# Performance work log

Measured on AMD Instinct MI355X. Metric: run time of the kernel, lower is better.

The kernel has to match this reference:

```python
import jax, jax.numpy as jnp
import numpy as np

N = 100000   # nodes
E = 3200000  # edges
CIN = 6
H = 256
G = 16       # graphs in batch
EPS = 1e-5


def setup_inputs() -> dict:
    key = jax.random.key(0)
    ks = jax.random.split(key, 16)
    inp = {
        'pos': jax.random.normal(ks[0], (N, 3), dtype=jnp.float32),
        'norm': jax.random.normal(ks[1], (N, 3), dtype=jnp.float32),
        'edge_index': jax.random.randint(ks[2], (2, E), 0, N, dtype=jnp.int64),
        'batch': jnp.sort(jax.random.randint(ks[3], (N,), 0, G, dtype=jnp.int64)),
        'bn0_g': jnp.ones((CIN,), jnp.float32), 'bn0_b': jnp.zeros((CIN,), jnp.float32),
    }
    dims = [(CIN, H), (H, H), (H, H), (H, H)]
    for i, (ci, co) in enumerate(dims, start=1):
        inp[f'W{i}'] = jax.random.normal(ks[3 + i], (ci, co), jnp.float32) * 0.05
        inp[f'b{i}'] = jnp.zeros((co,), jnp.float32)
        inp[f'bn{i}_g'] = jnp.ones((co,), jnp.float32)
        inp[f'bn{i}_b'] = jnp.zeros((co,), jnp.float32)
    return inp


def _bn(x, g, b):
    # BatchNorm1d, training mode: biased batch stats over node dim
    m = jnp.mean(x, axis=0)
    v = jnp.var(x, axis=0)
    return (x - m) * jax.lax.rsqrt(v + EPS) * g + b


def _gcn(x, W, bias, row, col, en, sl):
    # GCNConv: linear -> symmetric-normalized aggregation (with self loops) -> +bias
    xw = x @ W                                             # [N, C_out]
    agg = jax.ops.segment_sum(en[:, None] * xw[row], col, num_segments=N)
    return agg + sl[:, None] * xw + bias


def reference(pos, norm, edge_index, batch,
              bn0_g, bn0_b,
              W1, b1, bn1_g, bn1_b,
              W2, b2, bn2_g, bn2_b,
              W3, b3, bn3_g, bn3_b,
              W4, b4, bn4_g, bn4_b):
    row, col = edge_index[0], edge_index[1]
    # gcn_norm with self loops: deg includes +1 self loop weight
    deg = jax.ops.segment_sum(jnp.ones((E,), jnp.float32), col, num_segments=N) + 1.0
    dinv = jax.lax.rsqrt(deg)
    en = dinv[row] * dinv[col]   # edge norm
    sl = dinv * dinv             # self-loop norm

    x = jnp.concatenate([pos, norm], axis=1)   # [N, 6]
    x = _bn(x, bn0_g, bn0_b)
    for (W, b, g, be) in [(W1, b1, bn1_g, bn1_b), (W2, b2, bn2_g, bn2_b),
                          (W3, b3, bn3_g, bn3_b), (W4, b4, bn4_g, bn4_b)]:
        x = _bn(jax.nn.relu(_gcn(x, W, b, row, col, en, sl)), g, be)

    # global mean pool over graph ids
    sums = jax.ops.segment_sum(x, batch, num_segments=G)
    cnt = jax.ops.segment_sum(jnp.ones((N,), jnp.float32), batch, num_segments=G)
    return sums / jnp.maximum(cnt, 1.0)[:, None]
```

## Files before the change

kernel.cpp:

```cpp
#include <hip/hip_runtime.h>
#include <hip/hip_bf16.h>
#include <cstdint>

#define N_NODES 100000
#define NPAD    100032
#define N_EDGES 3200000
#define HID 256
#define NG 16
#define BN_EPS 1e-5f
#define B0 120
#define PB 1024
#define SROWS ((N_NODES + PB - 1) / PB)
#define PBR 128
#define RPR (PB / PBR)
#define FPART 25000
#define LDSROW 264

typedef unsigned short u16;
using bf16x8 = __attribute__((ext_vector_type(8))) short;
using f32x4  = __attribute__((ext_vector_type(4))) float;

__device__ __forceinline__ float bf2f(u16 b) {
    return __uint_as_float(((unsigned)b) << 16);
}
__device__ __forceinline__ u16 f2bf(float f) {
    unsigned u = __float_as_uint(f);
    unsigned r = (u + 0x7FFFu + ((u >> 16) & 1u)) >> 16;
    return (u16)r;
}
__device__ __forceinline__ float4 ld_bf16x4(const u16* p) {
    ushort4 u = *reinterpret_cast<const ushort4*>(p);
    float4 f;
    f.x = bf2f(u.x); f.y = bf2f(u.y); f.z = bf2f(u.z); f.w = bf2f(u.w);
    return f;
}

__global__ void k_count(const int* __restrict__ coli, int* __restrict__ cnt) {
    int i = blockIdx.x * blockDim.x + threadIdx.x;
    int st = gridDim.x * blockDim.x;
    for (; i < N_EDGES; i += st) atomicAdd(&cnt[coli[i]], 1);
}

__global__ void k_scan(const int* __restrict__ cnt, int* __restrict__ ptr,
                       int* __restrict__ ptr2, float* __restrict__ dinv) {
    __shared__ int wsum[16];
    const int t = threadIdx.x;
    const int wv = t >> 6;
    const int ln = t & 63;
    int carry = 0;
    for (int base = 0; base < N_NODES; base += 4096) {
        int idx = base + t * 4;
        int v0 = 0, v1 = 0, v2 = 0, v3 = 0;
        if (idx + 3 < N_NODES) {
            int4 q = *reinterpret_cast<const int4*>(&cnt[idx]);
            v0 = q.x; v1 = q.y; v2 = q.z; v3 = q.w;
        } else {
            if (idx + 0 < N_NODES) v0 = cnt[idx + 0];
            if (idx + 1 < N_NODES) v1 = cnt[idx + 1];
            if (idx + 2 < N_NODES) v2 = cnt[idx + 2];
        }
        if (idx + 0 < N_NODES) dinv[idx + 0] = rsqrtf((float)v0 + 1.0f);
        if (idx + 1 < N_NODES) dinv[idx + 1] = rsqrtf((float)v1 + 1.0f);
        if (idx + 2 < N_NODES) dinv[idx + 2] = rsqrtf((float)v2 + 1.0f);
        if (idx + 3 < N_NODES) dinv[idx + 3] = rsqrtf((float)v3 + 1.0f);
        int s = v0 + v1 + v2 + v3;
        int sc = s;
        for (int off = 1; off < 64; off <<= 1) {
            int u = __shfl_up(sc, off);
            if (ln >= off) sc += u;
        }
        if (ln == 63) wsum[wv] = sc;
        __syncthreads();
        if (wv == 0 && ln < 16) {
            int a = wsum[ln];
            for (int off = 1; off < 16; off <<= 1) {
                int u = __shfl_up(a, off, 16);
                if (ln >= off) a += u;
            }
            wsum[ln] = a;
        }
        __syncthreads();
        int total = wsum[15];
        int excl = carry + (wv ? wsum[wv - 1] : 0) + sc - s;
        if (idx + 0 < N_NODES) { ptr[idx + 0] = excl; ptr2[idx + 0] = excl; } excl += v0;
        if (idx + 1 < N_NODES) { ptr[idx + 1] = excl; ptr2[idx + 1] = excl; } excl += v1;
        if (idx + 2 < N_NODES) { ptr[idx + 2] = excl; ptr2[idx + 2] = excl; } excl += v2;
        if (idx + 3 < N_NODES) { ptr[idx + 3] = excl; ptr2[idx + 3] = excl; }
        __syncthreads();
        carry += total;
    }
    if (t == 0) ptr[N_NODES] = carry;
}

__global__ void k_fillp(const int* __restrict__ rowi, const int* __restrict__ coli,
                        int* __restrict__ ptr2, int* __restrict__ esrc, int lo) {
    int i = blockIdx.x * blockDim.x + threadIdx.x;
    int st = gridDim.x * blockDim.x;
    const int hi = lo + FPART;
    for (; i < N_EDGES; i += st) {
        int c = coli[i];
        if (c >= lo && c < hi) {
            int r = rowi[i];
            int p = atomicAdd(&ptr2[c], 1);
            esrc[p] = r;
        }
    }
}

__global__ __launch_bounds__(256) void k_bn0stats(const float* __restrict__ pos,
                                                  const float* __restrict__ nrm,
                                                  const int* __restrict__ batch,
                                                  float* __restrict__ part ,
                                                  int* __restrict__ cg) {
    __shared__ int h[NG];
    if (threadIdx.x < NG) h[threadIdx.x] = 0;
    __syncthreads();
    float s[6] = {0, 0, 0, 0, 0, 0}, q[6] = {0, 0, 0, 0, 0, 0};
    int i = blockIdx.x * blockDim.x + threadIdx.x;
    int stp = gridDim.x * blockDim.x;
    for (; i < N_NODES; i += stp) {
        float v;
        v = pos[i * 3 + 0]; s[0] += v; q[0] += v * v;
        v = pos[i * 3 + 1]; s[1] += v; q[1] += v * v;
        v = pos[i * 3 + 2]; s[2] += v; q[2] += v * v;
        v = nrm[i * 3 + 0]; s[3] += v; q[3] += v * v;
        v = nrm[i * 3 + 1]; s[4] += v; q[4] += v * v;
        v = nrm[i * 3 + 2]; s[5] += v; q[5] += v * v;
        atomicAdd(&h[batch[i]], 1);
    }
#pragma unroll
    for (int k = 0; k < 6; ++k) {
        for (int o = 32; o > 0; o >>= 1) { s[k] += __shfl_down(s[k], o); q[k] += __shfl_down(q[k], o); }
    }
    __shared__ float ls[4][12];
    const int wv = threadIdx.x >> 6;
    const int ln = threadIdx.x & 63;
    if (ln == 0) {
#pragma unroll
        for (int k = 0; k < 6; ++k) { ls[wv][k] = s[k]; ls[wv][6 + k] = q[k]; }
    }
    __syncthreads();
    if (threadIdx.x < 12)
        part[blockIdx.x * 12 + threadIdx.x] =
            ls[0][threadIdx.x] + ls[1][threadIdx.x] + ls[2][threadIdx.x] + ls[3][threadIdx.x];
    if (threadIdx.x < NG) {
        int v = h[threadIdx.x];
        if (v) atomicAdd(&cg[threadIdx.x], v);
    }
}

__global__ void k_fold6(const float* __restrict__ W,
                        const float* __restrict__ part, float invcnt,
                        const float* __restrict__ gamma, const float* __restrict__ beta,
                        float* __restrict__ Wf, float* __restrict__ rvB) {
    __shared__ float st[12];
    int c = threadIdx.x;
    if (c < 12) {
        float a = 0.f;
        for (int b = 0; b < B0; ++b) a += part[b * 12 + c];
        st[c] = a;
    }
    __syncthreads();
    float acc = 0.f;
    for (int k = 0; k < 6; ++k) {
        float m = st[k] * invcnt;
        float var = st[6 + k] * invcnt - m * m;
        float A = gamma[k] * rsqrtf(var + BN_EPS);
        float B = beta[k] - m * A;
        float w = W[k * HID + c];
        Wf[k * HID + c] = A * w;
        acc = fmaf(B, w, acc);
    }
    rvB[c] = acc;
}

__global__ __launch_bounds__(256) void k_reduce(const float* __restrict__ part,
                                                float* __restrict__ red) {
    const int b = blockIdx.x;
    const int t = threadIdx.x;
    float a0 = 0.f, a1 = 0.f;
#pragma unroll
    for (int r = 0; r < RPR; ++r) {
        const float* p = &part[(size_t)(b * RPR + r) * 512];
        a0 += p[t];
        a1 += p[t + 256];
    }
    red[(size_t)b * 512 + t] = a0;
    red[(size_t)b * 512 + 256 + t] = a1;
}

__global__ void k_fold256(const float* __restrict__ W,
                          const float* __restrict__ red , float invcnt,
                          const float* __restrict__ gamma, const float* __restrict__ beta,
                          u16* __restrict__ WhiT, u16* __restrict__ WloT,
                          float* __restrict__ rv) {
    __shared__ float ss[HID], sq[HID];
    int c = threadIdx.x;
    {
        float a = 0.f, b = 0.f;
#pragma unroll 4
        for (int bb = 0; bb < PBR; ++bb) {
            a += red[bb * 512 + c];
            b += red[bb * 512 + HID + c];
        }
        ss[c] = a; sq[c] = b;
    }
    __syncthreads();
    float acc = 0.f;
    for (int k = 0; k < HID; ++k) {
        float m = ss[k] * invcnt;
        float var = sq[k] * invcnt - m * m;
        float A = gamma[k] * rsqrtf(var + BN_EPS);
        float B = beta[k] - m * A;
        float w = W[k * HID + c];
        float wf = A * w;
        u16 hi = f2bf(wf);
        WhiT[c * HID + k] = hi;
        WloT[c * HID + k] = f2bf(wf - bf2f(hi));
        acc = fmaf(B, w, acc);
    }
    rv[c] = acc;
}

__global__ __launch_bounds__(256) void k_l1fused(
    const float* __restrict__ pos, const float* __restrict__ nrm,
    const int* __restrict__ ptr, const int* __restrict__ esrc,
    const float* __restrict__ dinv, const float* __restrict__ Wf,
    const float* __restrict__ rvB, const float* __restrict__ b1,
    u16* __restrict__ out) {
    const int wv = threadIdx.x >> 6;
    const int ln = threadIdx.x & 63;
    float w[6][4], rv4[4], bb4[4];
#pragma unroll
    for (int k = 0; k < 6; ++k) {
        float4 t = *reinterpret_cast<const float4*>(&Wf[k * HID + ln * 4]);
        w[k][0] = t.x; w[k][1] = t.y; w[k][2] = t.z; w[k][3] = t.w;
    }
    {
        float4 t = *reinterpret_cast<const float4*>(&rvB[ln * 4]);
        rv4[0] = t.x; rv4[1] = t.y; rv4[2] = t.z; rv4[3] = t.w;
        float4 u = *reinterpret_cast<const float4*>(&b1[ln * 4]);
        bb4[0] = u.x; bb4[1] = u.y; bb4[2] = u.z; bb4[3] = u.w;
    }
    for (int n = blockIdx.x * 4 + wv; n < N_NODES; n += gridDim.x * 4) {
        const float dn = dinv[n];
        float z0 = 0, z1 = 0, z2 = 0, z3 = 0, z4 = 0, z5 = 0, t = 0;
        const int s_ = ptr[n], e_ = ptr[n + 1];
        for (int e = s_ + ln; e < e_; e += 64) {
            int src = esrc[e];
            float we = dn * dinv[src];
            z0 = fmaf(we, pos[src * 3 + 0], z0);
            z1 = fmaf(we, pos[src * 3 + 1], z1);
            z2 = fmaf(we, pos[src * 3 + 2], z2);
            z3 = fmaf(we, nrm[src * 3 + 0], z3);
            z4 = fmaf(we, nrm[src * 3 + 1], z4);
            z5 = fmaf(we, nrm[src * 3 + 2], z5);
            t += we;
        }
        if (ln == 0) {
            float sl = dn * dn;
            z0 = fmaf(sl, pos[n * 3 + 0], z0);
            z1 = fmaf(sl, pos[n * 3 + 1], z1);
            z2 = fmaf(sl, pos[n * 3 + 2], z2);
            z3 = fmaf(sl, nrm[n * 3 + 0], z3);
            z4 = fmaf(sl, nrm[n * 3 + 1], z4);
            z5 = fmaf(sl, nrm[n * 3 + 2], z5);
            t += sl;
        }
#pragma unroll
        for (int o = 1; o < 64; o <<= 1) {
            z0 += __shfl_xor(z0, o); z1 += __shfl_xor(z1, o); z2 += __shfl_xor(z2, o);
            z3 += __shfl_xor(z3, o); z4 += __shfl_xor(z4, o); z5 += __shfl_xor(z5, o);
            t  += __shfl_xor(t, o);
        }
        ushort4 o4;
        float oj;
        oj = fmaf(t, rv4[0], bb4[0]);
        oj = fmaf(z0, w[0][0], oj); oj = fmaf(z1, w[1][0], oj); oj = fmaf(z2, w[2][0], oj);
        oj = fmaf(z3, w[3][0], oj); oj = fmaf(z4, w[4][0], oj); oj = fmaf(z5, w[5][0], oj);
        o4.x = f2bf(fmaxf(oj, 0.f));
        oj = fmaf(t, rv4[1], bb4[1]);
        oj = fmaf(z0, w[0][1], oj); oj = fmaf(z1, w[1][1], oj); oj = fmaf(z2, w[2][1], oj);
        oj = fmaf(z3, w[3][1], oj); oj = fmaf(z4, w[4][1], oj); oj = fmaf(z5, w[5][1], oj);
        o4.y = f2bf(fmaxf(oj, 0.f));
        oj = fmaf(t, rv4[2], bb4[2]);
        oj = fmaf(z0, w[0][2], oj); oj = fmaf(z1, w[1][2], oj); oj = fmaf(z2, w[2][2], oj);
        oj = fmaf(z3, w[3][2], oj); oj = fmaf(z4, w[4][2], oj); oj = fmaf(z5, w[5][2], oj);
        o4.z = f2bf(fmaxf(oj, 0.f));
        oj = fmaf(t, rv4[3], bb4[3]);
        oj = fmaf(z0, w[0][3], oj); oj = fmaf(z1, w[1][3], oj); oj = fmaf(z2, w[2][3], oj);
        oj = fmaf(z3, w[3][3], oj); oj = fmaf(z4, w[4][3], oj); oj = fmaf(z5, w[5][3], oj);
        o4.w = f2bf(fmaxf(oj, 0.f));
        *reinterpret_cast<ushort4*>(&out[(size_t)n * HID + ln * 4]) = o4;
    }
}

__global__ __launch_bounds__(256) void k_gemm_lds(
    const u16* __restrict__ X, const u16* __restrict__ WhiT,
    const u16* __restrict__ WloT, const float* __restrict__ rv,
    u16* __restrict__ out) {
    __shared__ u16 As[64 * LDSROW];
    const int tid = threadIdx.x;
    const int wv = tid >> 6;
    const int ln = tid & 63;
    const int row0 = blockIdx.x * 64;
    const int lr = ln & 15;
    const int lk = (ln >> 4) * 8;
    const int wcol0 = wv * 64;

#pragma unroll
    for (int i = 0; i < 8; ++i) {
        int chunk = i * 256 + tid;
        int r = chunk >> 5;
        int kc = chunk & 31;
        bf16x8 v = *reinterpret_cast<const bf16x8*>(&X[(size_t)(row0 + r) * HID + kc * 8]);
        *reinterpret_cast<bf16x8*>(&As[r * LDSROW + kc * 8]) = v;
    }
    __syncthreads();

    f32x4 acc[4][4] = {};
    for (int kk = 0; kk < HID; kk += 32) {
        bf16x8 a[4], bh[4], bl[4];
#pragma unroll
        for (int i = 0; i < 4; ++i)
            a[i] = *reinterpret_cast<const bf16x8*>(&As[(i * 16 + lr) * LDSROW + kk + lk]);
#pragma unroll
        for (int c = 0; c < 4; ++c) {
            int col = wcol0 + c * 16 + lr;
            bh[c] = *reinterpret_cast<const bf16x8*>(&WhiT[(size_t)col * HID + kk + lk]);
            bl[c] = *reinterpret_cast<const bf16x8*>(&WloT[(size_t)col * HID + kk + lk]);
        }
#pragma unroll
        for (int i = 0; i < 4; ++i)
#pragma unroll
            for (int c = 0; c < 4; ++c) {
                acc[i][c] = __builtin_amdgcn_mfma_f32_16x16x32_bf16(a[i], bh[c], acc[i][c], 0, 0, 0);
                acc[i][c] = __builtin_amdgcn_mfma_f32_16x16x32_bf16(a[i], bl[c], acc[i][c], 0, 0, 0);
            }
    }
    const int crow = (ln >> 4) * 4;
#pragma unroll
    for (int c = 0; c < 4; ++c) {
        int col = wcol0 + c * 16 + lr;
        float rvc = rv[col];
#pragma unroll
        for (int i = 0; i < 4; ++i) {
#pragma unroll
            for (int rg = 0; rg < 4; ++rg) {
                int r = row0 + i * 16 + crow + rg;
                out[(size_t)r * HID + col] = f2bf(acc[i][c][rg] + rvc);
            }
        }
    }
}

__global__ __launch_bounds__(256) void k_agg(
    const u16* __restrict__ xw, const int* __restrict__ ptr,
    const int* __restrict__ esrc, const float* __restrict__ dinv,
    const float* __restrict__ bias, u16* __restrict__ y) {
    const int wv = threadIdx.x >> 6;
    const int ln = threadIdx.x & 63;
    const int n = blockIdx.x * 4 + wv;
    const float dn = dinv[n];
    const size_t base = (size_t)n * HID + ln * 4;
    float4 v = ld_bf16x4(&xw[base]);
    const float sl = dn * dn;
    float a0 = v.x * sl, a1 = v.y * sl, a2 = v.z * sl, a3 = v.w * sl;
    const int s = ptr[n], e = ptr[n + 1];
    for (int bs = s; bs < e; bs += 64) {
        const int cnt = (e - bs < 64) ? e - bs : 64;
        int myidx = 0;
        float myw = 0.f;
        if (ln < cnt) {
            myidx = esrc[bs + ln];
            myw = dinv[myidx] * dn;
        }
        int j = 0;
        for (; j + 7 < cnt; j += 8) {
            int   s0 = __shfl(myidx, j),     s1 = __shfl(myidx, j + 1);
            int   s2 = __shfl(myidx, j + 2), s3 = __shfl(myidx, j + 3);
            int   s4 = __shfl(myidx, j + 4), s5 = __shfl(myidx, j + 5);
            int   s6 = __shfl(myidx, j + 6), s7 = __shfl(myidx, j + 7);
            float w0 = __shfl(myw, j),       w1 = __shfl(myw, j + 1);
            float w2 = __shfl(myw, j + 2),   w3 = __shfl(myw, j + 3);
            float w4 = __shfl(myw, j + 4),   w5 = __shfl(myw, j + 5);
            float w6 = __shfl(myw, j + 6),   w7 = __shfl(myw, j + 7);
            float4 u0 = ld_bf16x4(&xw[(size_t)s0 * HID + ln * 4]);
            float4 u1 = ld_bf16x4(&xw[(size_t)s1 * HID + ln * 4]);
            float4 u2 = ld_bf16x4(&xw[(size_t)s2 * HID + ln * 4]);
            float4 u3 = ld_bf16x4(&xw[(size_t)s3 * HID + ln * 4]);
            float4 u4 = ld_bf16x4(&xw[(size_t)s4 * HID + ln * 4]);
            float4 u5 = ld_bf16x4(&xw[(size_t)s5 * HID + ln * 4]);
            float4 u6 = ld_bf16x4(&xw[(size_t)s6 * HID + ln * 4]);
            float4 u7 = ld_bf16x4(&xw[(size_t)s7 * HID + ln * 4]);
            a0 = fmaf(w0, u0.x, a0); a1 = fmaf(w0, u0.y, a1);
            a2 = fmaf(w0, u0.z, a2); a3 = fmaf(w0, u0.w, a3);
            a0 = fmaf(w1, u1.x, a0); a1 = fmaf(w1, u1.y, a1);
            a2 = fmaf(w1, u1.z, a2); a3 = fmaf(w1, u1.w, a3);
            a0 = fmaf(w2, u2.x, a0); a1 = fmaf(w2, u2.y, a1);
            a2 = fmaf(w2, u2.z, a2); a3 = fmaf(w2, u2.w, a3);
            a0 = fmaf(w3, u3.x, a0); a1 = fmaf(w3, u3.y, a1);
            a2 = fmaf(w3, u3.z, a2); a3 = fmaf(w3, u3.w, a3);
            a0 = fmaf(w4, u4.x, a0); a1 = fmaf(w4, u4.y, a1);
            a2 = fmaf(w4, u4.z, a2); a3 = fmaf(w4, u4.w, a3);
            a0 = fmaf(w5, u5.x, a0); a1 = fmaf(w5, u5.y, a1);
            a2 = fmaf(w5, u5.z, a2); a3 = fmaf(w5, u5.w, a3);
            a0 = fmaf(w6, u6.x, a0); a1 = fmaf(w6, u6.y, a1);
            a2 = fmaf(w6, u6.z, a2); a3 = fmaf(w6, u6.w, a3);
            a0 = fmaf(w7, u7.x, a0); a1 = fmaf(w7, u7.y, a1);
            a2 = fmaf(w7, u7.z, a2); a3 = fmaf(w7, u7.w, a3);
        }
        for (; j < cnt; ++j) {
            int   s0 = __shfl(myidx, j);
            float w0 = __shfl(myw, j);
            float4 u0 = ld_bf16x4(&xw[(size_t)s0 * HID + ln * 4]);
            a0 = fmaf(w0, u0.x, a0); a1 = fmaf(w0, u0.y, a1);
            a2 = fmaf(w0, u0.z, a2); a3 = fmaf(w0, u0.w, a3);
        }
    }
    float4 b = *reinterpret_cast<const float4*>(&bias[ln * 4]);
    a0 = fmaxf(a0 + b.x, 0.f);
    a1 = fmaxf(a1 + b.y, 0.f);
    a2 = fmaxf(a2 + b.z, 0.f);
    a3 = fmaxf(a3 + b.w, 0.f);
    ushort4 o;
    o.x = f2bf(a0); o.y = f2bf(a1); o.z = f2bf(a2); o.w = f2bf(a3);
    *reinterpret_cast<ushort4*>(&y[base]) = o;
}

__global__ __launch_bounds__(256) void k_stats(const u16* __restrict__ y,
                                               float* __restrict__ part ) {
    const int t = threadIdx.x;
    const int cl = t & 63;
    const int rp = t >> 6;
    const int n0 = blockIdx.x * SROWS;
    const int n1 = (n0 + SROWS < N_NODES) ? n0 + SROWS : N_NODES;
    float s0 = 0, s1 = 0, s2 = 0, s3 = 0, q0 = 0, q1 = 0, q2 = 0, q3 = 0;
    for (int n = n0 + rp; n < n1; n += 4) {
        float4 v = ld_bf16x4(&y[(size_t)n * HID + cl * 4]);
        s0 += v.x; q0 = fmaf(v.x, v.x, q0);
        s1 += v.y; q1 = fmaf(v.y, v.y, q1);
        s2 += v.z; q2 = fmaf(v.z, v.z, q2);
        s3 += v.w; q3 = fmaf(v.w, v.w, q3);
    }
    __shared__ float sh[4 * 512];
    float* shr = &sh[rp * 512];
    shr[cl * 4 + 0] = s0; shr[cl * 4 + 1] = s1;
    shr[cl * 4 + 2] = s2; shr[cl * 4 + 3] = s3;
    shr[256 + cl * 4 + 0] = q0; shr[256 + cl * 4 + 1] = q1;
    shr[256 + cl * 4 + 2] = q2; shr[256 + cl * 4 + 3] = q3;
    __syncthreads();
    float a = sh[t] + sh[512 + t] + sh[1024 + t] + sh[1536 + t];
    float b = sh[256 + t] + sh[768 + t] + sh[1280 + t] + sh[1792 + t];
    part[blockIdx.x * 512 + t] = a;
    part[blockIdx.x * 512 + 256 + t] = b;
}

__global__ __launch_bounds__(256) void k_statspool(const u16* __restrict__ y,
                                                   const int* __restrict__ batch,
                                                   float* __restrict__ part,
                                                   float* __restrict__ ps) {
    const int c = threadIdx.x;
    const int n0 = blockIdx.x * SROWS;
    const int n1 = (n0 + SROWS < N_NODES) ? n0 + SROWS : N_NODES;
    float s = 0.f, q = 0.f;
    if (n0 < N_NODES) {
        int cur = batch[n0];
        float acc = 0.f;
        for (int n = n0; n < n1; ++n) {
            float v = bf2f(y[(size_t)n * HID + c]);
            int g = batch[n];
            if (g != cur) {
                atomicAdd(&ps[cur * HID + c], acc);
                acc = 0.f;
                cur = g;
            }
            s += v;
            q = fmaf(v, v, q);
            acc += v;
        }
        atomicAdd(&ps[cur * HID + c], acc);
    }
    part[blockIdx.x * 512 + c] = s;
    part[blockIdx.x * 512 + HID + c] = q;
}

__global__ void k_final(const float* __restrict__ ps, const int* __restrict__ cg,
                        const float* __restrict__ red, const float* __restrict__ gamma,
                        const float* __restrict__ beta, float* __restrict__ out) {
    __shared__ float ss[HID], sq[HID];
    const int c = threadIdx.x;
    {
        float a = 0.f, b = 0.f;
#pragma unroll 4
        for (int bb = 0; bb < PBR; ++bb) {
            a += red[bb * 512 + c];
            b += red[bb * 512 + HID + c];
        }
        ss[c] = a; sq[c] = b;
    }
    __syncthreads();
    const float invn = 1.0f / (float)N_NODES;
    float m = ss[c] * invn;
    float var = sq[c] * invn - m * m;
    float A = gamma[c] * rsqrtf(var + BN_EPS);
    float B = beta[c] - m * A;
    for (int g = 0; g < NG; ++g) {
        float cn = (float)cg[g];
        float val = (A * ps[g * HID + c] + cn * B) / fmaxf(cn, 1.0f);
        out[g * HID + c] = val;
    }
}

extern "C" void kernel_launch(void* const* d_in, const int* in_sizes, int n_in,
                              void* d_out, int out_size, void* d_ws, size_t ws_size,
                              hipStream_t stream) {
    const float* pos   = (const float*)d_in[0];
    const float* nrm   = (const float*)d_in[1];
    const int*   ei    = (const int*)d_in[2];
    const int*   batch = (const int*)d_in[3];
    const float* bn0g  = (const float*)d_in[4];
    const float* bn0b  = (const float*)d_in[5];
    const float* W[4]   = {(const float*)d_in[6],  (const float*)d_in[10], (const float*)d_in[14], (const float*)d_in[18]};
    const float* bb[4]  = {(const float*)d_in[7],  (const float*)d_in[11], (const float*)d_in[15], (const float*)d_in[19]};
    const float* bg[4]  = {(const float*)d_in[8],  (const float*)d_in[12], (const float*)d_in[16], (const float*)d_in[20]};
    const float* bbt[4] = {(const float*)d_in[9],  (const float*)d_in[13], (const float*)d_in[17], (const float*)d_in[21]};

    char* wp = (char*)d_ws;
    auto alloc = [&](size_t bytes) {
        char* p = wp;
        wp += (bytes + 255) & ~(size_t)255;
        return p;
    };
    float* dinv  = (float*)alloc((size_t)N_NODES * 4);
    int*   cnt   = (int*)  alloc((size_t)N_NODES * 4);
    int*   ptr   = (int*)  alloc((size_t)(N_NODES + 1) * 4);
    int*   ptr2  = (int*)  alloc((size_t)N_NODES * 4);
    int*   esrc  = (int*)  alloc((size_t)N_EDGES * 4);
    u16*   bufA  = (u16*)  alloc((size_t)NPAD * HID * 2);
    u16*   bufB  = (u16*)  alloc((size_t)NPAD * HID * 2);
    float* part0 = (float*)alloc((size_t)B0 * 12 * 4);
    float* partL = (float*)alloc((size_t)PB * 512 * 4);
    float* red   = (float*)alloc((size_t)PBR * 512 * 4);
    float* Wf1   = (float*)alloc((size_t)6 * HID * 4);
    u16*   WhiT  = (u16*)  alloc((size_t)HID * HID * 2);
    u16*   WloT  = (u16*)  alloc((size_t)HID * HID * 2);
    float* rv    = (float*)alloc(HID * 4);
    float* psz   = (float*)alloc((size_t)(NG * HID + NG) * 4);
    float* ps    = psz;
    int*   cg    = (int*)(psz + NG * HID);
    (void)ws_size; (void)in_sizes; (void)n_in; (void)out_size;

    const int* rowi = ei;
    const int* coli = ei + N_EDGES;

    hipMemsetAsync(cnt, 0, (size_t)N_NODES * 4, stream);
    hipMemsetAsync(psz, 0, (size_t)(NG * HID + NG) * 4, stream);

    k_count<<<2048, 256, 0, stream>>>(coli, cnt);
    k_scan<<<1, 1024, 0, stream>>>(cnt, ptr, ptr2, dinv);
    for (int p = 0; p < 4; ++p)
        k_fillp<<<1024, 256, 0, stream>>>(rowi, coli, ptr2, esrc, p * FPART);

    k_bn0stats<<<B0, 256, 0, stream>>>(pos, nrm, batch, part0, cg);
    k_fold6<<<1, 256, 0, stream>>>(W[0], part0, 1.0f / (float)N_NODES, bn0g, bn0b, Wf1, rv);
    k_l1fused<<<2048, 256, 0, stream>>>(pos, nrm, ptr, esrc, dinv, Wf1, rv, bb[0], bufA);

    for (int l = 0; l < 3; ++l) {
        k_stats<<<PB, 256, 0, stream>>>(bufA, partL);
        k_reduce<<<PBR, 256, 0, stream>>>(partL, red);
        k_fold256<<<1, 256, 0, stream>>>(W[l + 1], red, 1.0f / (float)N_NODES,
                                         bg[l], bbt[l], WhiT, WloT, rv);
        k_gemm_lds<<<NPAD / 64, 256, 0, stream>>>(bufA, WhiT, WloT, rv, bufB);
        k_agg<<<N_NODES / 4, 256, 0, stream>>>(bufB, ptr, esrc, dinv, bb[l + 1], bufA);
    }

    k_statspool<<<PB, 256, 0, stream>>>(bufA, batch, partL, ps);
    k_reduce<<<PBR, 256, 0, stream>>>(partL, red);
    k_final<<<1, 256, 0, stream>>>(ps, cg, red, bg[3], bbt[3], (float*)d_out);
}
```

Baseline: 1.615 ms.

## Fuse BN statistics into aggregation kernels and parallelize the CSR scan

```diff
diff --git a/kernel.cpp b/kernel.cpp
--- a/kernel.cpp
+++ b/kernel.cpp
@@ -9,12 +9,12 @@
 #define NG 16
 #define BN_EPS 1e-5f
 #define B0 120
-#define PB 1024
-#define SROWS ((N_NODES + PB - 1) / PB)
-#define PBR 128
-#define RPR (PB / PBR)
+#define NB 391
+#define SLABS 128
 #define FPART 25000
 #define LDSROW 264
+#define AGB 2048
+#define NGRP (N_NODES / 4)
 
 typedef unsigned short u16;
 using bf16x8 = __attribute__((ext_vector_type(8))) short;
@@ -41,55 +41,55 @@
     for (; i < N_EDGES; i += st) atomicAdd(&cnt[coli[i]], 1);
 }
 
-__global__ void k_scan(const int* __restrict__ cnt, int* __restrict__ ptr,
-                       int* __restrict__ ptr2, float* __restrict__ dinv) {
-    __shared__ int wsum[16];
+__global__ __launch_bounds__(256) void k_scanA(const int* __restrict__ cnt,
+                                               int* __restrict__ bsum) {
     const int t = threadIdx.x;
-    const int wv = t >> 6;
-    const int ln = t & 63;
-    int carry = 0;
-    for (int base = 0; base < N_NODES; base += 4096) {
-        int idx = base + t * 4;
-        int v0 = 0, v1 = 0, v2 = 0, v3 = 0;
-        if (idx + 3 < N_NODES) {
-            int4 q = *reinterpret_cast<const int4*>(&cnt[idx]);
-            v0 = q.x; v1 = q.y; v2 = q.z; v3 = q.w;
-        } else {
-            if (idx + 0 < N_NODES) v0 = cnt[idx + 0];
-            if (idx + 1 < N_NODES) v1 = cnt[idx + 1];
-            if (idx + 2 < N_NODES) v2 = cnt[idx + 2];
-        }
-        if (idx + 0 < N_NODES) dinv[idx + 0] = rsqrtf((float)v0 + 1.0f);
-        if (idx + 1 < N_NODES) dinv[idx + 1] = rsqrtf((float)v1 + 1.0f);
-        if (idx + 2 < N_NODES) dinv[idx + 2] = rsqrtf((float)v2 + 1.0f);
-        if (idx + 3 < N_NODES) dinv[idx + 3] = rsqrtf((float)v3 + 1.0f);
-        int s = v0 + v1 + v2 + v3;
-        int sc = s;
-        for (int off = 1; off < 64; off <<= 1) {
-            int u = __shfl_up(sc, off);
-            if (ln >= off) sc += u;
-        }
-        if (ln == 63) wsum[wv] = sc;
-        __syncthreads();
-        if (wv == 0 && ln < 16) {
-            int a = wsum[ln];
-            for (int off = 1; off < 16; off <<= 1) {
-                int u = __shfl_up(a, off, 16);
-                if (ln >= off) a += u;
-            }
-            wsum[ln] = a;
-        }
-        __syncthreads();
-        int total = wsum[15];
-        int excl = carry + (wv ? wsum[wv - 1] : 0) + sc - s;
-        if (idx + 0 < N_NODES) { ptr[idx + 0] = excl; ptr2[idx + 0] = excl; } excl += v0;
-        if (idx + 1 < N_NODES) { ptr[idx + 1] = excl; ptr2[idx + 1] = excl; } excl += v1;
-        if (idx + 2 < N_NODES) { ptr[idx + 2] = excl; ptr2[idx + 2] = excl; } excl += v2;
-        if (idx + 3 < N_NODES) { ptr[idx + 3] = excl; ptr2[idx + 3] = excl; }
-        __syncthreads();
-        carry += total;
-    }
-    if (t == 0) ptr[N_NODES] = carry;
+    const int i = blockIdx.x * 256 + t;
+    int v = (i < N_NODES) ? cnt[i] : 0;
+    for (int o = 32; o > 0; o >>= 1) v += __shfl_down(v, o);
+    __shared__ int ws[4];
+    if ((t & 63) == 0) ws[t >> 6] = v;
+    __syncthreads();
+    if (t == 0) bsum[blockIdx.x] = ws[0] + ws[1] + ws[2] + ws[3];
+}
+
+__global__ __launch_bounds__(512) void k_scanB(const int* __restrict__ bsum,
+                                               int* __restrict__ boff,
+                                               int* __restrict__ ptrN) {
+    const int t = threadIdx.x;
+    const int ln = t & 63, wv = t >> 6;
+    int v = (t < NB) ? bsum[t] : 0;
+    int sc = v;
+    for (int o = 1; o < 64; o <<= 1) { int u = __shfl_up(sc, o); if (ln >= o) sc += u; }
+    __shared__ int ws[8], wx[9];
+    if (ln == 63) ws[wv] = sc;
+    __syncthreads();
+    if (t == 0) { int a = 0; for (int k = 0; k < 8; ++k) { wx[k] = a; a += ws[k]; } wx[8] = a; }
+    __syncthreads();
+    int excl = wx[wv] + sc - v;
+    if (t < NB) boff[t] = excl;
+    if (t == 0) ptrN[0] = wx[8];
+}
+
+__global__ __launch_bounds__(256) void k_scanC(const int* __restrict__ cnt,
+                                               const int* __restrict__ boff,
+                                               int* __restrict__ ptr,
+                                               int* __restrict__ ptr2,
+                                               float* __restrict__ dinv) {
+    const int t = threadIdx.x;
+    const int i = blockIdx.x * 256 + t;
+    const int ln = t & 63, wv = t >> 6;
+    int v = (i < N_NODES) ? cnt[i] : 0;
+    if (i < N_NODES) dinv[i] = rsqrtf((float)v + 1.0f);
+    int sc = v;
+    for (int o = 1; o < 64; o <<= 1) { int u = __shfl_up(sc, o); if (ln >= o) sc += u; }
+    __shared__ int ws[4], wx[4];
+    if (ln == 63) ws[wv] = sc;
+    __syncthreads();
+    if (t == 0) { int a = 0; for (int k = 0; k < 4; ++k) { wx[k] = a; a += ws[k]; } }
+    __syncthreads();
+    int excl = boff[blockIdx.x] + wx[wv] + sc - v;
+    if (i < N_NODES) { ptr[i] = excl; ptr2[i] = excl; }
 }
 
 __global__ void k_fillp(const int* __restrict__ rowi, const int* __restrict__ coli,
@@ -174,23 +174,8 @@
     rvB[c] = acc;
 }
 
-__global__ __launch_bounds__(256) void k_reduce(const float* __restrict__ part,
-                                                float* __restrict__ red) {
-    const int b = blockIdx.x;
-    const int t = threadIdx.x;
-    float a0 = 0.f, a1 = 0.f;
-#pragma unroll
-    for (int r = 0; r < RPR; ++r) {
-        const float* p = &part[(size_t)(b * RPR + r) * 512];
-        a0 += p[t];
-        a1 += p[t + 256];
-    }
-    red[(size_t)b * 512 + t] = a0;
-    red[(size_t)b * 512 + 256 + t] = a1;
-}
-
 __global__ void k_fold256(const float* __restrict__ W,
-                          const float* __restrict__ red , float invcnt,
+                          const float* __restrict__ partL , float invcnt,
                           const float* __restrict__ gamma, const float* __restrict__ beta,
                           u16* __restrict__ WhiT, u16* __restrict__ WloT,
                           float* __restrict__ rv) {
@@ -199,9 +184,9 @@
     {
         float a = 0.f, b = 0.f;
 #pragma unroll 4
-        for (int bb = 0; bb < PBR; ++bb) {
-            a += red[bb * 512 + c];
-            b += red[bb * 512 + HID + c];
+        for (int bb = 0; bb < SLABS; ++bb) {
+            a += partL[bb * 512 + c];
+            b += partL[bb * 512 + HID + c];
         }
         ss[c] = a; sq[c] = b;
     }
@@ -227,7 +212,7 @@
     const int* __restrict__ ptr, const int* __restrict__ esrc,
     const float* __restrict__ dinv, const float* __restrict__ Wf,
     const float* __restrict__ rvB, const float* __restrict__ b1,
-    u16* __restrict__ out) {
+    u16* __restrict__ out, float* __restrict__ partL) {
     const int wv = threadIdx.x >> 6;
     const int ln = threadIdx.x & 63;
     float w[6][4], rv4[4], bb4[4];
@@ -242,7 +227,8 @@
         float4 u = *reinterpret_cast<const float4*>(&b1[ln * 4]);
         bb4[0] = u.x; bb4[1] = u.y; bb4[2] = u.z; bb4[3] = u.w;
     }
-    for (int n = blockIdx.x * 4 + wv; n < N_NODES; n += gridDim.x * 4) {
+    float ssr[4] = {0, 0, 0, 0}, qqr[4] = {0, 0, 0, 0};
+    for (int n = blockIdx.x * 4 + wv; n < N_NODES; n += AGB * 4) {
         const float dn = dinv[n];
         float z0 = 0, z1 = 0, z2 = 0, z3 = 0, z4 = 0, z5 = 0, t = 0;
         const int s_ = ptr[n], e_ = ptr[n + 1];
@@ -274,25 +260,28 @@
             t  += __shfl_xor(t, o);
         }
         ushort4 o4;
-        float oj;
-        oj = fmaf(t, rv4[0], bb4[0]);
-        oj = fmaf(z0, w[0][0], oj); oj = fmaf(z1, w[1][0], oj); oj = fmaf(z2, w[2][0], oj);
-        oj = fmaf(z3, w[3][0], oj); oj = fmaf(z4, w[4][0], oj); oj = fmaf(z5, w[5][0], oj);
-        o4.x = f2bf(fmaxf(oj, 0.f));
-        oj = fmaf(t, rv4[1], bb4[1]);
-        oj = fmaf(z0, w[0][1], oj); oj = fmaf(z1, w[1][1], oj); oj = fmaf(z2, w[2][1], oj);
-        oj = fmaf(z3, w[3][1], oj); oj = fmaf(z4, w[4][1], oj); oj = fmaf(z5, w[5][1], oj);
-        o4.y = f2bf(fmaxf(oj, 0.f));
-        oj = fmaf(t, rv4[2], bb4[2]);
-        oj = fmaf(z0, w[0][2], oj); oj = fmaf(z1, w[1][2], oj); oj = fmaf(z2, w[2][2], oj);
-        oj = fmaf(z3, w[3][2], oj); oj = fmaf(z4, w[4][2], oj); oj = fmaf(z5, w[5][2], oj);
-        o4.z = f2bf(fmaxf(oj, 0.f));
-        oj = fmaf(t, rv4[3], bb4[3]);
-        oj = fmaf(z0, w[0][3], oj); oj = fmaf(z1, w[1][3], oj); oj = fmaf(z2, w[2][3], oj);
-        oj = fmaf(z3, w[3][3], oj); oj = fmaf(z4, w[4][3], oj); oj = fmaf(z5, w[5][3], oj);
-        o4.w = f2bf(fmaxf(oj, 0.f));
+#pragma unroll
+        for (int j = 0; j < 4; ++j) {
+            float oj = fmaf(t, rv4[j], bb4[j]);
+            oj = fmaf(z0, w[0][j], oj); oj = fmaf(z1, w[1][j], oj); oj = fmaf(z2, w[2][j], oj);
+            oj = fmaf(z3, w[3][j], oj); oj = fmaf(z4, w[4][j], oj); oj = fmaf(z5, w[5][j], oj);
+            oj = fmaxf(oj, 0.f);
+            ssr[j] += oj; qqr[j] = fmaf(oj, oj, qqr[j]);
+            ((u16*)&o4)[j] = f2bf(oj);
+        }
         *reinterpret_cast<ushort4*>(&out[(size_t)n * HID + ln * 4]) = o4;
     }
+    __shared__ float sh[4 * 512];
+    float* shw = &sh[wv * 512];
+#pragma unroll
+    for (int j = 0; j < 4; ++j) { shw[ln * 4 + j] = ssr[j]; shw[256 + ln * 4 + j] = qqr[j]; }
+    __syncthreads();
+    const int t = threadIdx.x;
+    float S = sh[t] + sh[512 + t] + sh[1024 + t] + sh[1536 + t];
+    float Q = sh[256 + t] + sh[768 + t] + sh[1280 + t] + sh[1792 + t];
+    float* slab = &partL[(size_t)(blockIdx.x & (SLABS - 1)) * 512];
+    atomicAdd(&slab[t], S);
+    atomicAdd(&slab[256 + t], Q);
 }
 
 __global__ __launch_bounds__(256) void k_gemm_lds(
@@ -357,145 +346,113 @@
 __global__ __launch_bounds__(256) void k_agg(
     const u16* __restrict__ xw, const int* __restrict__ ptr,
     const int* __restrict__ esrc, const float* __restrict__ dinv,
-    const float* __restrict__ bias, u16* __restrict__ y) {
+    const float* __restrict__ bias, u16* __restrict__ y,
+    float* __restrict__ partL) {
     const int wv = threadIdx.x >> 6;
     const int ln = threadIdx.x & 63;
-    const int n = blockIdx.x * 4 + wv;
-    const float dn = dinv[n];
-    const size_t base = (size_t)n * HID + ln * 4;
-    float4 v = ld_bf16x4(&xw[base]);
-    const float sl = dn * dn;
-    float a0 = v.x * sl, a1 = v.y * sl, a2 = v.z * sl, a3 = v.w * sl;
-    const int s = ptr[n], e = ptr[n + 1];
-    for (int bs = s; bs < e; bs += 64) {
-        const int cnt = (e - bs < 64) ? e - bs : 64;
-        int myidx = 0;
-        float myw = 0.f;
-        if (ln < cnt) {
-            myidx = esrc[bs + ln];
-            myw = dinv[myidx] * dn;
-        }
-        int j = 0;
-        for (; j + 7 < cnt; j += 8) {
-            int   s0 = __shfl(myidx, j),     s1 = __shfl(myidx, j + 1);
-            int   s2 = __shfl(myidx, j + 2), s3 = __shfl(myidx, j + 3);
-            int   s4 = __shfl(myidx, j + 4), s5 = __shfl(myidx, j + 5);
-            int   s6 = __shfl(myidx, j + 6), s7 = __shfl(myidx, j + 7);
-            float w0 = __shfl(myw, j),       w1 = __shfl(myw, j + 1);
-            float w2 = __shfl(myw, j + 2),   w3 = __shfl(myw, j + 3);
-            float w4 = __shfl(myw, j + 4),   w5 = __shfl(myw, j + 5);
-            float w6 = __shfl(myw, j + 6),   w7 = __shfl(myw, j + 7);
-            float4 u0 = ld_bf16x4(&xw[(size_t)s0 * HID + ln * 4]);
-            float4 u1 = ld_bf16x4(&xw[(size_t)s1 * HID + ln * 4]);
-            float4 u2 = ld_bf16x4(&xw[(size_t)s2 * HID + ln * 4]);
-            float4 u3 = ld_bf16x4(&xw[(size_t)s3 * HID + ln * 4]);
-            float4 u4 = ld_bf16x4(&xw[(size_t)s4 * HID + ln * 4]);
-            float4 u5 = ld_bf16x4(&xw[(size_t)s5 * HID + ln * 4]);
-            float4 u6 = ld_bf16x4(&xw[(size_t)s6 * HID + ln * 4]);
-            float4 u7 = ld_bf16x4(&xw[(size_t)s7 * HID + ln * 4]);
-            a0 = fmaf(w0, u0.x, a0); a1 = fmaf(w0, u0.y, a1);
-            a2 = fmaf(w0, u0.z, a2); a3 = fmaf(w0, u0.w, a3);
-            a0 = fmaf(w1, u1.x, a0); a1 = fmaf(w1, u1.y, a1);
-            a2 = fmaf(w1, u1.z, a2); a3 = fmaf(w1, u1.w, a3);
-            a0 = fmaf(w2, u2.x, a0); a1 = fmaf(w2, u2.y, a1);
-            a2 = fmaf(w2, u2.z, a2); a3 = fmaf(w2, u2.w, a3);
-            a0 = fmaf(w3, u3.x, a0); a1 = fmaf(w3, u3.y, a1);
-            a2 = fmaf(w3, u3.z, a2); a3 = fmaf(w3, u3.w, a3);
-            a0 = fmaf(w4, u4.x, a0); a1 = fmaf(w4, u4.y, a1);
-            a2 = fmaf(w4, u4.z, a2); a3 = fmaf(w4, u4.w, a3);
-            a0 = fmaf(w5, u5.x, a0); a1 = fmaf(w5, u5.y, a1);
-            a2 = fmaf(w5, u5.z, a2); a3 = fmaf(w5, u5.w, a3);
-            a0 = fmaf(w6, u6.x, a0); a1 = fmaf(w6, u6.y, a1);
-            a2 = fmaf(w6, u6.z, a2); a3 = fmaf(w6, u6.w, a3);
-            a0 = fmaf(w7, u7.x, a0); a1 = fmaf(w7, u7.y, a1);
-            a2 = fmaf(w7, u7.z, a2); a3 = fmaf(w7, u7.w, a3);
-        }
-        for (; j < cnt; ++j) {
-            int   s0 = __shfl(myidx, j);
-            float w0 = __shfl(myw, j);
-            float4 u0 = ld_bf16x4(&xw[(size_t)s0 * HID + ln * 4]);
-            a0 = fmaf(w0, u0.x, a0); a1 = fmaf(w0, u0.y, a1);
-            a2 = fmaf(w0, u0.z, a2); a3 = fmaf(w0, u0.w, a3);
-        }
-    }
     float4 b = *reinterpret_cast<const float4*>(&bias[ln * 4]);
-    a0 = fmaxf(a0 + b.x, 0.f);
-    a1 = fmaxf(a1 + b.y, 0.f);
-    a2 = fmaxf(a2 + b.z, 0.f);
-    a3 = fmaxf(a3 + b.w, 0.f);
-    ushort4 o;
-    o.x = f2bf(a0); o.y = f2bf(a1); o.z = f2bf(a2); o.w = f2bf(a3);
-    *reinterpret_cast<ushort4*>(&y[base]) = o;
-}
-
-__global__ __launch_bounds__(256) void k_stats(const u16* __restrict__ y,
-                                               float* __restrict__ part ) {
+    float ssr[4] = {0, 0, 0, 0}, qqr[4] = {0, 0, 0, 0};
+    for (int g = blockIdx.x; g < NGRP; g += AGB) {
+        const int n = g * 4 + wv;
+        const float dn = dinv[n];
+        const size_t base = (size_t)n * HID + ln * 4;
+        float4 v = ld_bf16x4(&xw[base]);
+        const float sl = dn * dn;
+        float a0 = v.x * sl, a1 = v.y * sl, a2 = v.z * sl, a3 = v.w * sl;
+        const int s = ptr[n], e = ptr[n + 1];
+        for (int bs = s; bs < e; bs += 64) {
+            const int cnt = (e - bs < 64) ? e - bs : 64;
+            int myidx = 0;
+            float myw = 0.f;
+            if (ln < cnt) {
+                myidx = esrc[bs + ln];
+                myw = dinv[myidx] * dn;
+            }
+            int j = 0;
+            for (; j + 3 < cnt; j += 4) {
+                int   s0 = __shfl(myidx, j),     s1 = __shfl(myidx, j + 1);
+                int   s2 = __shfl(myidx, j + 2), s3 = __shfl(myidx, j + 3);
+                float w0 = __shfl(myw, j),       w1 = __shfl(myw, j + 1);
+                float w2 = __shfl(myw, j + 2),   w3 = __shfl(myw, j + 3);
+                float4 u0 = ld_bf16x4(&xw[(size_t)s0 * HID + ln * 4]);
+                float4 u1 = ld_bf16x4(&xw[(size_t)s1 * HID + ln * 4]);
+                float4 u2 = ld_bf16x4(&xw[(size_t)s2 * HID + ln * 4]);
+                float4 u3 = ld_bf16x4(&xw[(size_t)s3 * HID + ln * 4]);
+                a0 = fmaf(w0, u0.x, a0); a1 = fmaf(w0, u0.y, a1);
+                a2 = fmaf(w0, u0.z, a2); a3 = fmaf(w0, u0.w, a3);
+                a0 = fmaf(w1, u1.x, a0); a1 = fmaf(w1, u1.y, a1);
+                a2 = fmaf(w1, u1.z, a2); a3 = fmaf(w1, u1.w, a3);
+                a0 = fmaf(w2, u2.x, a0); a1 = fmaf(w2, u2.y, a1);
+                a2 = fmaf(w2, u2.z, a2); a3 = fmaf(w2, u2.w, a3);
+                a0 = fmaf(w3, u3.x, a0); a1 = fmaf(w3, u3.y, a1);
+                a2 = fmaf(w3, u3.z, a2); a3 = fmaf(w3, u3.w, a3);
+            }
+            for (; j < cnt; ++j) {
+                int   s0 = __shfl(myidx, j);
+                float w0 = __shfl(myw, j);
+                float4 u0 = ld_bf16x4(&xw[(size_t)s0 * HID + ln * 4]);
+                a0 = fmaf(w0, u0.x, a0); a1 = fmaf(w0, u0.y, a1);
+                a2 = fmaf(w0, u0.z, a2); a3 = fmaf(w0, u0.w, a3);
+            }
+        }
+        a0 = fmaxf(a0 + b.x, 0.f);
+        a1 = fmaxf(a1 + b.y, 0.f);
+        a2 = fmaxf(a2 + b.z, 0.f);
+        a3 = fmaxf(a3 + b.w, 0.f);
+        ssr[0] += a0; qqr[0] = fmaf(a0, a0, qqr[0]);
+        ssr[1] += a1; qqr[1] = fmaf(a1, a1, qqr[1]);
+        ssr[2] += a2; qqr[2] = fmaf(a2, a2, qqr[2]);
+        ssr[3] += a3; qqr[3] = fmaf(a3, a3, qqr[3]);
+        ushort4 o;
+        o.x = f2bf(a0); o.y = f2bf(a1); o.z = f2bf(a2); o.w = f2bf(a3);
+        *reinterpret_cast<ushort4*>(&y[base]) = o;
+    }
+    __shared__ float sh[4 * 512];
+    float* shw = &sh[wv * 512];
+#pragma unroll
+    for (int j = 0; j < 4; ++j) { shw[ln * 4 + j] = ssr[j]; shw[256 + ln * 4 + j] = qqr[j]; }
+    __syncthreads();
     const int t = threadIdx.x;
-    const int cl = t & 63;
-    const int rp = t >> 6;
-    const int n0 = blockIdx.x * SROWS;
-    const int n1 = (n0 + SROWS < N_NODES) ? n0 + SROWS : N_NODES;
-    float s0 = 0, s1 = 0, s2 = 0, s3 = 0, q0 = 0, q1 = 0, q2 = 0, q3 = 0;
-    for (int n = n0 + rp; n < n1; n += 4) {
-        float4 v = ld_bf16x4(&y[(size_t)n * HID + cl * 4]);
-        s0 += v.x; q0 = fmaf(v.x, v.x, q0);
-        s1 += v.y; q1 = fmaf(v.y, v.y, q1);
-        s2 += v.z; q2 = fmaf(v.z, v.z, q2);
-        s3 += v.w; q3 = fmaf(v.w, v.w, q3);
-    }
-    __shared__ float sh[4 * 512];
-    float* shr = &sh[rp * 512];
-    shr[cl * 4 + 0] = s0; shr[cl * 4 + 1] = s1;
-    shr[cl * 4 + 2] = s2; shr[cl * 4 + 3] = s3;
-    shr[256 + cl * 4 + 0] = q0; shr[256 + cl * 4 + 1] = q1;
-    shr[256 + cl * 4 + 2] = q2; shr[256 + cl * 4 + 3] = q3;
-    __syncthreads();
-    float a = sh[t] + sh[512 + t] + sh[1024 + t] + sh[1536 + t];
-    float b = sh[256 + t] + sh[768 + t] + sh[1280 + t] + sh[1792 + t];
-    part[blockIdx.x * 512 + t] = a;
-    part[blockIdx.x * 512 + 256 + t] = b;
-}
-
-__global__ __launch_bounds__(256) void k_statspool(const u16* __restrict__ y,
-                                                   const int* __restrict__ batch,
-                                                   float* __restrict__ part,
-                                                   float* __restrict__ ps) {
+    float S = sh[t] + sh[512 + t] + sh[1024 + t] + sh[1536 + t];
+    float Q = sh[256 + t] + sh[768 + t] + sh[1280 + t] + sh[1792 + t];
+    float* slab = &partL[(size_t)(blockIdx.x & (SLABS - 1)) * 512];
+    atomicAdd(&slab[t], S);
+    atomicAdd(&slab[256 + t], Q);
+}
+
+__global__ __launch_bounds__(256) void k_pool(const u16* __restrict__ y,
+                                              const int* __restrict__ batch,
+                                              float* __restrict__ ps) {
     const int c = threadIdx.x;
-    const int n0 = blockIdx.x * SROWS;
-    const int n1 = (n0 + SROWS < N_NODES) ? n0 + SROWS : N_NODES;
-    float s = 0.f, q = 0.f;
-    if (n0 < N_NODES) {
-        int cur = batch[n0];
-        float acc = 0.f;
-        for (int n = n0; n < n1; ++n) {
-            float v = bf2f(y[(size_t)n * HID + c]);
-            int g = batch[n];
-            if (g != cur) {
-                atomicAdd(&ps[cur * HID + c], acc);
-                acc = 0.f;
-                cur = g;
-            }
-            s += v;
-            q = fmaf(v, v, q);
-            acc += v;
-        }
-        atomicAdd(&ps[cur * HID + c], acc);
-    }
-    part[blockIdx.x * 512 + c] = s;
-    part[blockIdx.x * 512 + HID + c] = q;
+    const int n0 = blockIdx.x * 98;
+    if (n0 >= N_NODES) return;
+    const int n1 = (n0 + 98 < N_NODES) ? n0 + 98 : N_NODES;
+    int cur = batch[n0];
+    float acc = 0.f;
+    for (int n = n0; n < n1; ++n) {
+        float v = bf2f(y[(size_t)n * HID + c]);
+        int g = batch[n];
+        if (g != cur) {
+            atomicAdd(&ps[cur * HID + c], acc);
+            acc = 0.f;
+            cur = g;
+        }
+        acc += v;
+    }
+    atomicAdd(&ps[cur * HID + c], acc);
 }
 
 __global__ void k_final(const float* __restrict__ ps, const int* __restrict__ cg,
-                        const float* __restrict__ red, const float* __restrict__ gamma,
+                        const float* __restrict__ partL, const float* __restrict__ gamma,
                         const float* __restrict__ beta, float* __restrict__ out) {
     __shared__ float ss[HID], sq[HID];
     const int c = threadIdx.x;
     {
         float a = 0.f, b = 0.f;
 #pragma unroll 4
-        for (int bb = 0; bb < PBR; ++bb) {
-            a += red[bb * 512 + c];
-            b += red[bb * 512 + HID + c];
+        for (int bb = 0; bb < SLABS; ++bb) {
+            a += partL[bb * 512 + c];
+            b += partL[bb * 512 + HID + c];
         }
         ss[c] = a; sq[c] = b;
     }
@@ -537,11 +494,12 @@
     int*   ptr   = (int*)  alloc((size_t)(N_NODES + 1) * 4);
     int*   ptr2  = (int*)  alloc((size_t)N_NODES * 4);
     int*   esrc  = (int*)  alloc((size_t)N_EDGES * 4);
+    int*   bsum  = (int*)  alloc((size_t)NB * 4);
+    int*   boff  = (int*)  alloc((size_t)NB * 4);
     u16*   bufA  = (u16*)  alloc((size_t)NPAD * HID * 2);
     u16*   bufB  = (u16*)  alloc((size_t)NPAD * HID * 2);
     float* part0 = (float*)alloc((size_t)B0 * 12 * 4);
-    float* partL = (float*)alloc((size_t)PB * 512 * 4);
-    float* red   = (float*)alloc((size_t)PBR * 512 * 4);
+    float* partL = (float*)alloc((size_t)SLABS * 512 * 4);
     float* Wf1   = (float*)alloc((size_t)6 * HID * 4);
     u16*   WhiT  = (u16*)  alloc((size_t)HID * HID * 2);
     u16*   WloT  = (u16*)  alloc((size_t)HID * HID * 2);
@@ -556,26 +514,27 @@
 
     hipMemsetAsync(cnt, 0, (size_t)N_NODES * 4, stream);
     hipMemsetAsync(psz, 0, (size_t)(NG * HID + NG) * 4, stream);
+    hipMemsetAsync(partL, 0, (size_t)SLABS * 512 * 4, stream);
 
     k_count<<<2048, 256, 0, stream>>>(coli, cnt);
-    k_scan<<<1, 1024, 0, stream>>>(cnt, ptr, ptr2, dinv);
+    k_scanA<<<NB, 256, 0, stream>>>(cnt, bsum);
+    k_scanB<<<1, 512, 0, stream>>>(bsum, boff, &ptr[N_NODES]);
+    k_scanC<<<NB, 256, 0, stream>>>(cnt, boff, ptr, ptr2, dinv);
     for (int p = 0; p < 4; ++p)
         k_fillp<<<1024, 256, 0, stream>>>(rowi, coli, ptr2, esrc, p * FPART);
 
     k_bn0stats<<<B0, 256, 0, stream>>>(pos, nrm, batch, part0, cg);
     k_fold6<<<1, 256, 0, stream>>>(W[0], part0, 1.0f / (float)N_NODES, bn0g, bn0b, Wf1, rv);
-    k_l1fused<<<2048, 256, 0, stream>>>(pos, nrm, ptr, esrc, dinv, Wf1, rv, bb[0], bufA);
+    k_l1fused<<<AGB, 256, 0, stream>>>(pos, nrm, ptr, esrc, dinv, Wf1, rv, bb[0], bufA, partL);
 
     for (int l = 0; l < 3; ++l) {
-        k_stats<<<PB, 256, 0, stream>>>(bufA, partL);
-        k_reduce<<<PBR, 256, 0, stream>>>(partL, red);
-        k_fold256<<<1, 256, 0, stream>>>(W[l + 1], red, 1.0f / (float)N_NODES,
+        k_fold256<<<1, 256, 0, stream>>>(W[l + 1], partL, 1.0f / (float)N_NODES,
                                          bg[l], bbt[l], WhiT, WloT, rv);
+        hipMemsetAsync(partL, 0, (size_t)SLABS * 512 * 4, stream);
         k_gemm_lds<<<NPAD / 64, 256, 0, stream>>>(bufA, WhiT, WloT, rv, bufB);
-        k_agg<<<N_NODES / 4, 256, 0, stream>>>(bufB, ptr, esrc, dinv, bb[l + 1], bufA);
-    }
-
-    k_statspool<<<PB, 256, 0, stream>>>(bufA, batch, partL, ps);
-    k_reduce<<<PBR, 256, 0, stream>>>(partL, red);
-    k_final<<<1, 256, 0, stream>>>(ps, cg, red, bg[3], bbt[3], (float*)d_out);
-}
+        k_agg<<<AGB, 256, 0, stream>>>(bufB, ptr, esrc, dinv, bb[l + 1], bufA, partL);
+    }
+
+    k_pool<<<(N_NODES + 97) / 98, 256, 0, stream>>>(bufA, batch, ps);
+    k_final<<<1, 256, 0, stream>>>(ps, cg, partL, bg[3], bbt[3], (float*)d_out);
+}
```

After: 1.580 ms. 2.2% less time.
